# Kernel tuning notes

Hardware: AMD Instinct MI355X
Metric: run time of the kernel (lower is better)

## Reference

```python
import jax, jax.numpy as jnp
import numpy as np


def _conv(x, w, b=None, stride=1, pad=1, groups=1):
    y = jax.lax.conv_general_dilated(
        x, w, (stride, stride), [(pad, pad), (pad, pad)],
        dimension_numbers=('NCHW', 'OIHW', 'NCHW'), feature_group_count=groups)
    return y if b is None else y + b[None, :, None, None]


def _dwt(x):
    # Haar DWT as grouped stride-2 conv, filters pre-flipped as in the torch code
    ll = np.array([[0.5, 0.5], [0.5, 0.5]])
    lh = np.array([[-0.5, -0.5], [0.5, 0.5]])
    hl = np.array([[-0.5, 0.5], [-0.5, 0.5]])
    hh = np.array([[0.5, -0.5], [-0.5, 0.5]])
    filts = np.stack([f[None, ::-1, ::-1] for f in (ll, lh, hl, hh)], 0)  # [4,1,2,2]
    w = jnp.asarray(np.concatenate([filts] * 3, 0), x.dtype)  # [12,1,2,2], groups=3
    return _conv(x, w, None, stride=2, pad=0, groups=3)


def setup_inputs():
    key = jax.random.key(0)
    ks = iter(jax.random.split(key, 64))
    def w(*shape):
        return jax.random.normal(next(ks), shape, jnp.float32) * 0.05
    B, H, W = 4, 512, 512
    F = 32  # number_f
    d = {'x': jax.random.uniform(next(ks), (B, 3, H, W), jnp.float32)}
    d['enc1_w'] = w(F, 3, 3, 3); d['enc1_b'] = w(F)
    for i in range(2, 6):
        d['enc%d_w' % i] = w(F, F, 3, 3); d['enc%d_b' % i] = w(F)
    d['cdc_w'] = w(F, F, 3, 3)                      # central-difference conv, no bias
    d['ct_w'] = w(64, 9, 3, 3); d['ct_b'] = w(64)   # conv_theta on 9-ch high_freq
    d['t1_w'] = w(64, 64, 1, 1); d['t1_b'] = w(64)
    d['t2_w'] = w(64, 64, 1, 1); d['t2_b'] = w(64)
    d['t3_w'] = w(1, 64, 1, 1); d['t3_b'] = w(1)
    d['lf_w'] = w(64, 3, 3, 3); d['lf_b'] = w(64)   # low_freq conv on haar_A
    d['fc1_w'] = w(512, 64); d['fc1_b'] = w(512)
    d['fc2_w'] = w(512, 512); d['fc2_b'] = w(512)
    d['fc3_w'] = w(512, 512); d['fc3_b'] = w(512)
    d['g_w'] = w(F, 512); d['g_b'] = w(F)           # to_gamma_0
    d['be_w'] = w(F, 512); d['be_b'] = w(F)         # to_beta_0
    d['res_w'] = w(F, F, 3, 3); d['res_b'] = w(F)
    d['d1_w'] = w(F, F, 3, 3); d['d1_b'] = w(F)
    d['d2_w'] = w(1, F, 3, 3); d['d2_b'] = w(1)
    return d


def reference(x, enc1_w, enc1_b, enc2_w, enc2_b, enc3_w, enc3_b, enc4_w, enc4_b,
              enc5_w, enc5_b, cdc_w, ct_w, ct_b, t1_w, t1_b, t2_w, t2_b, t3_w, t3_b,
              lf_w, lf_b, fc1_w, fc1_b, fc2_w, fc2_b, fc3_w, fc3_b,
              g_w, g_b, be_w, be_b, res_w, res_b, d1_w, d1_b, d2_w, d2_b):
    relu = jax.nn.relu
    # encoder
    f = relu(_conv(x, enc1_w, enc1_b))
    f = relu(_conv(f, enc2_w, enc2_b))
    f = relu(_conv(f, enc3_w, enc3_b))
    f = relu(_conv(f, enc4_w, enc4_b))
    f_org4 = relu(_conv(f, enc5_w, enc5_b))  # [B,32,H,W]
    # Haar wavelet split: per input channel blocks of 4 = (A,H,V,D)
    dwt = _dwt(x)                             # [B,12,H/2,W/2]
    haar_A = dwt[:, 0::4]                     # c1,c5,c9
    high_freq = jnp.concatenate([dwt[:, 1::4], dwt[:, 2::4], dwt[:, 3::4]], 1)  # [B,9,...]
    # theta net (Conv2d_cd)
    a = relu(_conv(high_freq, ct_w, ct_b))
    a = a.mean((2, 3), keepdims=True)         # adaptive avg pool to 1x1
    a = relu(_conv(a, t1_w, t1_b, pad=0))
    a = relu(_conv(a, t2_w, t2_b, pad=0))
    theta = jax.nn.sigmoid(_conv(a, t3_w, t3_b, pad=0))   # [B,1,1,1]
    out_normal = _conv(f_org4, cdc_w, None)
    kdiff = cdc_w.sum((2, 3))[:, :, None, None]            # [32,32,1,1]
    out_diff = _conv(f_org4, kdiff, None, pad=0)
    f_deco = relu(out_normal - theta * out_diff)           # [B,32,H,W]
    # attention / FiLM branch
    am = relu(_conv(haar_A, lf_w, lf_b)).mean((2, 3))      # [B,64]
    am = relu(am @ fc1_w.T + fc1_b)
    am = relu(am @ fc2_w.T + fc2_b)
    am = jax.nn.sigmoid(am @ fc3_w.T + fc3_b)              # [B,512]
    gamma = jax.nn.sigmoid(am @ g_w.T + g_b)[:, :, None, None]  # [B,32,1,1]
    beta = jnp.tanh(am @ be_w.T + be_b)[:, :, None, None]
    f = f_deco + gamma * _conv(f_deco, res_w, res_b) + beta
    # decoder
    f = relu(_conv(f, d1_w, d1_b))
    out_map = jnp.tanh(_conv(f, d2_w, d2_b))               # [B,1,H,W]
    enhance_image = x + out_map * (x * x - x)
    return enhance_image, out_map
```

## Files before the change

### kernel.cpp

```cpp
#include <hip/hip_runtime.h>
#include <hip/hip_bf16.h>
#include <cmath>

#define TPB 256

typedef __attribute__((ext_vector_type(8))) short s16x8;
typedef __attribute__((ext_vector_type(4))) float f32x4;
typedef unsigned short ushortT;

constexpr long long PSTR = 8454272;
constexpr int HW = 512 * 512;

static __device__ __forceinline__ short f2bf(float f) {
    union { __hip_bfloat16 h; short s; } u;
    u.h = __float2bfloat16(f);
    return u.s;
}
static __device__ __forceinline__ float bf2f(unsigned short u) {
    union { unsigned int i; float f; } v;
    v.i = ((unsigned int)u) << 16;
    return v.f;
}
static __device__ __forceinline__ unsigned int pack2(float a, float b) {
    return (unsigned int)(unsigned short)f2bf(a) | ((unsigned int)(unsigned short)f2bf(b) << 16);
}

#define GLOAD_LDS16(gp, lp) \
    __builtin_amdgcn_global_load_lds((const __attribute__((address_space(1))) void*)(gp), \
                                     (__attribute__((address_space(3))) void*)(lp), 16, 0, 0)

static __device__ void pack_body(const float* w, const float* bias, const float* theta,
                                 short* dst, int CO, int CI_src, int ci_off, int cog, int l)
{
    const int l15 = l & 15, sl = l >> 4;
    for (int t = 0; t < 9; ++t) {
        for (int mt = 0; mt < 2; ++mt) {
            const int co = cog * 32 + 16 * mt + l15;
            s16x8 p;
            #pragma unroll
            for (int i = 0; i < 8; ++i) {
                const int pci = 8 * sl + i;
                float val = 0.f;
                if (co < CO && pci >= ci_off && pci < ci_off + CI_src) {
                    const int ci = pci - ci_off;
                    val = w[((size_t)co * CI_src + ci) * 9 + t];
                    if (theta && t == 4) {
                        float s = 0.f;
                        for (int tt = 0; tt < 9; ++tt) s += w[((size_t)co * CI_src + ci) * 9 + tt];
                        val -= theta[0] * s;
                    }
                }
                p[i] = f2bf(val);
            }
            *(s16x8*)(dst + ((size_t)(t * 2 + mt) * 64 + l) * 8) = p;
        }
    }
    if (l < 32) {
        const int co = cog * 32 + l;
        ((float*)(dst + 9216))[l] = (bias && co < CO) ? bias[co] : 0.f;
    }
}

__global__ __launch_bounds__(64) void packall_k(
    const float* e1w, const float* e1b, const float* e2w, const float* e2b,
    const float* e3w, const float* e3b, const float* e4w, const float* e4b,
    const float* e5w, const float* e5b, const float* resw, const float* resb,
    const float* d1w, const float* d1b, const float* d2w, const float* d2b,
    const float* ctw, const float* ctb, const float* lfw, const float* lfb,
    short* wpack)
{
    const int s = blockIdx.x;
    const float *w, *b;
    int CO = 32, CI = 32, coff = 0, cog = 0;
    switch (s) {
        case 0: w = e1w; b = e1b; CI = 3; break;
        case 1: w = e2w; b = e2b; break;
        case 2: w = e3w; b = e3b; break;
        case 3: w = e4w; b = e4b; break;
        case 4: w = e5w; b = e5b; break;
        case 5: w = resw; b = resb; break;
        case 6: w = d1w; b = d1b; break;
        case 7: w = d2w; b = d2b; CO = 1; break;
        case 8: case 9: w = ctw; b = ctb; CO = 64; CI = 9; cog = s - 8; break;
        default: w = lfw; b = lfb; CO = 64; CI = 3; coff = 9; cog = s - 10; break;
    }
    pack_body(w, b, nullptr, wpack + (size_t)s * 10240, CO, CI, coff, cog, threadIdx.x);
}

__global__ __launch_bounds__(64) void packcdc_k(
    const float* cdcw, const float* theta, short* wpack)
{
    const int b = blockIdx.x;
    pack_body(cdcw, nullptr, theta + b, wpack + (size_t)(12 + b) * 10240, 32, 32, 0, 0, threadIdx.x);
}

__global__ __launch_bounds__(TPB) void zero_k(unsigned int* A2u, unsigned int* B2u)
{
    const int idx = blockIdx.x * TPB + threadIdx.x;
    if (idx >= 8 * 32832) return;
    const int q = idx / 32832, r = idx % 32832;
    unsigned int* P = (q < 4 ? A2u : B2u) + (size_t)(q & 3) * 4227136;
    const int RSU = 514 * 16;
    int off;
    if (r < 8224)       off = r;
    else if (r < 16448) off = 513 * RSU + (r - 8224);
    else if (r < 24640) { int u = r - 16448; off = (1 + (u >> 4)) * RSU + (u & 15); }
    else                { int u = r - 24640; off = (1 + (u >> 4)) * RSU + 513 * 16 + (u & 15); }
    P[off] = 0u;
}

__global__ __launch_bounds__(TPB) void ctlf_k(
    const float* __restrict__ hf0, const float* __restrict__ haarA0,
    const short* __restrict__ wpack8, float* __restrict__ part)
{
    constexpr int RSX = 66;
    constexpr int ROWB = RSX * 64;
    __shared__ s16x8 lds_t[6 * RSX * 4];
    __shared__ float s_red[4][32];
    char* sb = (char*)lds_t;

    const int z = blockIdx.z, cog = blockIdx.y;
    const int bid = blockIdx.x;
    const int x0 = (bid & 3) * 64, y0 = (bid >> 2) * 4;
    const int tid = threadIdx.x, lane = tid & 63, wv = tid >> 6;
    const int l15 = lane & 15, slot = lane >> 4;

    const short* wslot = wpack8 + (size_t)cog * 10240;
    const float* hfz = hf0 + (size_t)z * 9 * 65536;
    const float* haz = haarA0 + (size_t)z * 3 * 65536;

    s16x8 wf[9][2];
    #pragma unroll
    for (int t = 0; t < 9; ++t)
        #pragma unroll
        for (int mt = 0; mt < 2; ++mt)
            wf[t][mt] = *(const s16x8*)(wslot + ((size_t)(t * 2 + mt) * 64 + lane) * 8);

    #pragma unroll
    for (int j = 0; j < 7; ++j) {
        const int p = j * 256 + tid;
        if (p < 1584) {
            const int row = p / 264;
            const int rem = p - row * 264;
            const int lx = rem >> 2, osl = rem & 3;
            const int o = osl ^ ((lx + (lx >> 2)) & 3);
            s16x8 pk;
            #pragma unroll
            for (int i = 0; i < 8; ++i) pk[i] = 0;
            const int sy = y0 + row - 1, sx = x0 + lx - 1;
            if (o < 2 && sy >= 0 && sy < 256 && sx >= 0 && sx < 256) {
                const size_t base = (size_t)sy * 256 + sx;
                if (o == 0) {
                    #pragma unroll
                    for (int i = 0; i < 8; ++i)
                        pk[i] = f2bf(hfz[(size_t)i * 65536 + base]);
                } else {
                    pk[0] = f2bf(hfz[(size_t)8 * 65536 + base]);
                    pk[1] = f2bf(haz[base]);
                    pk[2] = f2bf(haz[(size_t)65536 + base]);
                    pk[3] = f2bf(haz[(size_t)2 * 65536 + base]);
                }
            }
            *(s16x8*)(sb + p * 16) = pk;
        }
    }
    __syncthreads();

    const int xw = 16 * wv;
    int roff[3];
    #pragma unroll
    for (int dx = 0; dx < 3; ++dx) {
        const int lx = xw + dx + l15;
        const int vs = (lx + (lx >> 2)) & 3;
        roff[dx] = lx * 64 + ((slot ^ vs) << 4);
    }
    const float* bptr = (const float*)(wslot + 9216);

    float ps[2][4];
    #pragma unroll
    for (int mt = 0; mt < 2; ++mt)
        #pragma unroll
        for (int reg = 0; reg < 4; ++reg) ps[mt][reg] = 0.f;

    #pragma unroll
    for (int r2 = 0; r2 < 4; r2 += 2) {
        f32x4 acc[2][2];
        #pragma unroll
        for (int a = 0; a < 2; ++a)
            #pragma unroll
            for (int b = 0; b < 2; ++b)
                #pragma unroll
                for (int e = 0; e < 4; ++e) acc[a][b][e] = 0.f;

        #pragma unroll
        for (int dy = 0; dy < 3; ++dy) {
            const int rb0 = (r2 + dy) * ROWB;
            #pragma unroll
            for (int dx = 0; dx < 3; ++dx) {
                const int tap = dy * 3 + dx;
                const s16x8 b0 = *(const s16x8*)(sb + rb0 + roff[dx]);
                const s16x8 b1 = *(const s16x8*)(sb + rb0 + ROWB + roff[dx]);
                #pragma unroll
                for (int mt = 0; mt < 2; ++mt) {
                    acc[0][mt] = __builtin_amdgcn_mfma_f32_16x16x32_bf16(wf[tap][mt], b0, acc[0][mt], 0, 0, 0);
                    acc[1][mt] = __builtin_amdgcn_mfma_f32_16x16x32_bf16(wf[tap][mt], b1, acc[1][mt], 0, 0, 0);
                }
            }
        }

        #pragma unroll
        for (int rr = 0; rr < 2; ++rr)
            #pragma unroll
            for (int mt = 0; mt < 2; ++mt)
                #pragma unroll
                for (int reg = 0; reg < 4; ++reg)
                    ps[mt][reg] += fmaxf(acc[rr][mt][reg] + bptr[16 * mt + 4 * slot + reg], 0.f);
    }

    #pragma unroll
    for (int mt = 0; mt < 2; ++mt)
        #pragma unroll
        for (int reg = 0; reg < 4; ++reg) {
            #pragma unroll
            for (int o = 1; o < 16; o <<= 1)
                ps[mt][reg] += __shfl_xor(ps[mt][reg], o, 64);
        }
    #pragma unroll
    for (int mt = 0; mt < 2; ++mt)
        #pragma unroll
        for (int reg = 0; reg < 4; ++reg)
            if (l15 == mt * 4 + reg)
                s_red[wv][16 * mt + 4 * slot + reg] = ps[mt][reg];
    __syncthreads();
    if (tid < 32) {
        const float s = s_red[0][tid] + s_red[1][tid] + s_red[2][tid] + s_red[3][tid];
        part[(((size_t)z * 4 + cog) * 256 + bid) * 32 + tid] = s;
    }
}

__global__ __launch_bounds__(TPB) void enc1n_k(
    const float* __restrict__ x0p, const short* __restrict__ wslot,
    ushortT* __restrict__ outP0)
{
    constexpr int RSX = 66;
    constexpr int ROWB = RSX * 64;
    __shared__ s16x8 lds_t[6 * RSX * 4];
    char* sb = (char*)lds_t;

    const int z = blockIdx.z;
    const float* xin = x0p + (size_t)z * 3 * HW;

    const int tid = threadIdx.x, lane = tid & 63, wv = tid >> 6;
    const int bid = blockIdx.x;
    const int swz = (bid & 7) * 128 + (bid >> 3);
    const int x0 = (swz & 7) * 64, y0 = (swz >> 3) * 4;
    const int l15 = lane & 15, slot = lane >> 4;

    s16x8 wf[9][2];
    #pragma unroll
    for (int t = 0; t < 9; ++t)
        #pragma unroll
        for (int mt = 0; mt < 2; ++mt)
            wf[t][mt] = *(const s16x8*)(wslot + ((size_t)(t * 2 + mt) * 64 + lane) * 8);

    #pragma unroll
    for (int j = 0; j < 7; ++j) {
        const int p = j * 256 + tid;
        if (p < 1584) {
            const int row = p / 264;
            const int rem = p - row * 264;
            const int lx = rem >> 2, osl = rem & 3;
            const int o = osl ^ ((lx + (lx >> 2)) & 3);
            s16x8 pk;
            #pragma unroll
            for (int i = 0; i < 8; ++i) pk[i] = 0;
            if (o == 0) {
                const int gy = y0 + row - 1;
                const int gx = x0 + lx - 1;
                if (gy >= 0 && gy < 512 && gx >= 0 && gx < 512) {
                    #pragma unroll
                    for (int c = 0; c < 3; ++c)
                        pk[c] = f2bf(xin[((size_t)c * 512 + gy) * 512 + gx]);
                }
            }
            *(s16x8*)(sb + p * 16) = pk;
        }
    }
    __syncthreads();

    const int xw = 16 * wv;
    int roff[3];
    #pragma unroll
    for (int dx = 0; dx < 3; ++dx) {
        const int lx = xw + dx + l15;
        const int vs = (lx + (lx >> 2)) & 3;
        roff[dx] = lx * 64 + ((slot ^ vs) << 4);
    }
    const float* bptr = (const float*)(wslot + 9216);
    ushortT* outP = outP0 + (size_t)z * PSTR;

    #pragma unroll
    for (int r2 = 0; r2 < 4; r2 += 2) {
        f32x4 acc[2][2];
        #pragma unroll
        for (int a = 0; a < 2; ++a)
            #pragma unroll
            for (int b = 0; b < 2; ++b)
                #pragma unroll
                for (int e = 0; e < 4; ++e) acc[a][b][e] = 0.f;

        #pragma unroll
        for (int dy = 0; dy < 3; ++dy) {
            const int rb0 = (r2 + dy) * ROWB;
            #pragma unroll
            for (int dx = 0; dx < 3; ++dx) {
                const int tap = dy * 3 + dx;
                const s16x8 b0 = *(const s16x8*)(sb + rb0 + roff[dx]);
                const s16x8 b1 = *(const s16x8*)(sb + rb0 + ROWB + roff[dx]);
                #pragma unroll
                for (int mt = 0; mt < 2; ++mt) {
                    acc[0][mt] = __builtin_amdgcn_mfma_f32_16x16x32_bf16(wf[tap][mt], b0, acc[0][mt], 0, 0, 0);
                    acc[1][mt] = __builtin_amdgcn_mfma_f32_16x16x32_bf16(wf[tap][mt], b1, acc[1][mt], 0, 0, 0);
                }
            }
        }

        #pragma unroll
        for (int rr = 0; rr < 2; ++rr) {
            const int gy = y0 + r2 + rr;
            const int gx = x0 + xw + l15;
            #pragma unroll
            for (int mt = 0; mt < 2; ++mt) {
                const size_t off = ((size_t)(gy + 1) * 514 + gx + 1) * 32 + 16 * mt + 4 * slot;
                float v[4];
                #pragma unroll
                for (int reg = 0; reg < 4; ++reg)
                    v[reg] = fmaxf(acc[rr][mt][reg] + bptr[16 * mt + 4 * slot + reg], 0.f);
                *(uint2*)(outP + off) = make_uint2(pack2(v[0], v[1]), pack2(v[2], v[3]));
            }
        }
    }
}

template<int EPI>
__global__ __launch_bounds__(TPB) void dconv64p_k(
    const ushortT* __restrict__ inP0, const short* __restrict__ wbase, int wstr,
    ushortT* __restrict__ outP0,
    const float* __restrict__ gamma0, const float* __restrict__ beta0,
    const float* __restrict__ xorig0, float* __restrict__ outE0, float* __restrict__ outM0)
{
    constexpr int MT = (EPI == 3) ? 1 : 2;
    constexpr int RSX = 66;
    constexpr int ROWB = RSX * 64;
    constexpr int BUFB = 6 * RSX * 64;
    __shared__ s16x8 lds_t[2 * 6 * RSX * 4];
    char* sbase = (char*)lds_t;

    const int z = blockIdx.z;
    const ushortT* inP = inP0 + (size_t)z * PSTR;
    const short* wslot = wbase + (size_t)z * wstr;

    const int tid = threadIdx.x, lane = tid & 63, wv = tid >> 6;
    const int bid = blockIdx.x;
    const int xcd = bid & 7, idx = bid >> 3;
    const int x0 = (idx & 7) * 64;
    const int yband = xcd * 4 + (idx >> 3);
    const int l15 = lane & 15, slot = lane >> 4;

    s16x8 wf[9][MT];
    #pragma unroll
    for (int t = 0; t < 9; ++t)
        #pragma unroll
        for (int mt = 0; mt < MT; ++mt)
            wf[t][mt] = *(const s16x8*)(wslot + ((size_t)(t * 2 + mt) * 64 + lane) * 8);

    const int xw = 16 * wv;
    int roff[3];
    #pragma unroll
    for (int dx = 0; dx < 3; ++dx) {
        const int lx = xw + dx + l15;
        const int vs = (lx + (lx >> 2)) & 3;
        roff[dx] = lx * 64 + ((slot ^ vs) << 4);
    }
    const float* bptr = (const float*)(wslot + 9216);

    auto stage = [&](int t, int b) {
        const int y0 = yband * 16 + 4 * t;
        char* sb = sbase + b * BUFB;
        #pragma unroll
        for (int j = 0; j < 6; ++j) {
            const int p = j * 256 + tid;
            const int row = p / 264;
            const int rem = p - row * 264;
            const int lx = rem >> 2, osl = rem & 3;
            const int o = osl ^ ((lx + (lx >> 2)) & 3);
            const ushortT* gp = inP + ((size_t)(y0 + row) * 514 + x0 + lx) * 32 + o * 8;
            GLOAD_LDS16(gp, sb + (size_t)(j * 256 + wv * 64) * 16);
        }
        if (tid < 48) {
            const int p = 1536 + tid;
            const int row = p / 264;
            const int rem = p - row * 264;
            const int lx = rem >> 2, osl = rem & 3;
            const int o = osl ^ ((lx + (lx >> 2)) & 3);
            const ushortT* gp = inP + ((size_t)(y0 + row) * 514 + x0 + lx) * 32 + o * 8;
            GLOAD_LDS16(gp, sb + (size_t)1536 * 16);
        }
    };

    stage(0, 0);

    #pragma unroll 1
    for (int t = 0; t < 4; ++t) {
        __syncthreads();
        if (t < 3) stage(t + 1, (t + 1) & 1);
        char* sb = sbase + (t & 1) * BUFB;
        const int y0t = yband * 16 + 4 * t;

        #pragma unroll
        for (int r2 = 0; r2 < 4; r2 += 2) {
            f32x4 acc[2][MT];
            #pragma unroll
            for (int a = 0; a < 2; ++a)
                #pragma unroll
                for (int b = 0; b < MT; ++b)
                    #pragma unroll
                    for (int e = 0; e < 4; ++e) acc[a][b][e] = 0.f;

            #pragma unroll
            for (int dy = 0; dy < 3; ++dy) {
                const int rb0 = (r2 + dy) * ROWB;
                #pragma unroll
                for (int dx = 0; dx < 3; ++dx) {
                    const int tap = dy * 3 + dx;
                    const s16x8 b0 = *(const s16x8*)(sb + rb0 + roff[dx]);
                    const s16x8 b1 = *(const s16x8*)(sb + rb0 + ROWB + roff[dx]);
                    #pragma unroll
                    for (int mt = 0; mt < MT; ++mt) {
                        acc[0][mt] = __builtin_amdgcn_mfma_f32_16x16x32_bf16(wf[tap][mt], b0, acc[0][mt], 0, 0, 0);
                        acc[1][mt] = __builtin_amdgcn_mfma_f32_16x16x32_bf16(wf[tap][mt], b1, acc[1][mt], 0, 0, 0);
                    }
                }
            }

            #pragma unroll
            for (int rr = 0; rr < 2; ++rr) {
                const int gy = y0t + r2 + rr;
                const int gx = x0 + xw + l15;
                if constexpr (EPI == 3) {
                    if (slot == 0) {
                        const float* xorig = xorig0 + (size_t)z * 3 * HW;
                        float* outE = outE0 + (size_t)z * 3 * HW;
                        float* outM = outM0 + (size_t)z * HW;
                        const float om = tanhf(acc[rr][0][0] + bptr[0]);
                        outM[(size_t)gy * 512 + gx] = om;
                        #pragma unroll
                        for (int c = 0; c < 3; ++c) {
                            const size_t xi = ((size_t)c * 512 + gy) * 512 + gx;
                            const float xv = xorig[xi];
                            outE[xi] = xv + om * (xv * xv - xv);
                        }
                    }
                } else {
                    ushortT* outP = outP0 + (size_t)z * PSTR;
                    #pragma unroll
                    for (int mt = 0; mt < MT; ++mt) {
                        const size_t off = ((size_t)(gy + 1) * 514 + gx + 1) * 32 + 16 * mt + 4 * slot;
                        float v[4];
                        #pragma unroll
                        for (int reg = 0; reg < 4; ++reg)
                            v[reg] = acc[rr][mt][reg] + bptr[16 * mt + 4 * slot + reg];
                        if constexpr (EPI == 0) {
                            #pragma unroll
                            for (int reg = 0; reg < 4; ++reg) v[reg] = fmaxf(v[reg], 0.f);
                        } else if constexpr (EPI == 2) {
                            const int prow = r2 + rr + 1;
                            const int lxr = xw + l15 + 1;
                            const int vsr = (lxr + (lxr >> 2)) & 3;
                            const int oo = (2 * mt + (slot >> 1)) ^ vsr;
                            const uint2 din = *(const uint2*)(sb + (prow * RSX + lxr) * 64 + (oo << 4) + ((slot & 1) << 3));
                            const float* gamma = gamma0 + 32 * z;
                            const float* beta  = beta0 + 32 * z;
                            const int cb = 16 * mt + 4 * slot;
                            v[0] = bf2f((unsigned short)(din.x & 0xffff)) + gamma[cb + 0] * v[0] + beta[cb + 0];
                            v[1] = bf2f((unsigned short)(din.x >> 16))    + gamma[cb + 1] * v[1] + beta[cb + 1];
                            v[2] = bf2f((unsigned short)(din.y & 0xffff)) + gamma[cb + 2] * v[2] + beta[cb + 2];
                            v[3] = bf2f((unsigned short)(din.y >> 16))    + gamma[cb + 3] * v[3] + beta[cb + 3];
                        }
                        *(uint2*)(outP + off) = make_uint2(pack2(v[0], v[1]), pack2(v[2], v[3]));
                    }
                }
            }
        }
    }
}

__global__ __launch_bounds__(TPB) void dwt_k(
    const float* __restrict__ x, float* __restrict__ haarA, float* __restrict__ hf)
{
    const int idx = blockIdx.x * TPB + threadIdx.x;
    if (idx >= 4 * 256 * 256) return;
    const int xo = idx & 255;
    const int yo = (idx >> 8) & 255;
    const int b  = idx >> 16;
    #pragma unroll
    for (int c = 0; c < 3; ++c) {
        const float* p = x + (((size_t)b * 3 + c) * 512 + 2 * yo) * 512 + 2 * xo;
        const float a = p[0], bb = p[1], cc = p[512], d = p[513];
        haarA[(((size_t)b * 3 + c) * 256 + yo) * 256 + xo] = 0.5f * (a + bb + cc + d);
        hf[(((size_t)b * 9 + 0 + c) * 256 + yo) * 256 + xo] = 0.5f * (a + bb - cc - d);
        hf[(((size_t)b * 9 + 3 + c) * 256 + yo) * 256 + xo] = 0.5f * (a - bb + cc - d);
        hf[(((size_t)b * 9 + 6 + c) * 256 + yo) * 256 + xo] = 0.5f * (a - bb - cc + d);
    }
}

__global__ __launch_bounds__(TPB) void meanfin_k(
    const float* __restrict__ part, float* __restrict__ amean, float* __restrict__ am0)
{
    const int br = blockIdx.x;
    const int o = threadIdx.x;
    const int z = o >> 6, co = o & 63;
    const int cog = (br ? 2 : 0) + (co >> 5), c = co & 31;
    const float* p = part + (((size_t)z * 4 + cog) * 256) * 32 + c;
    float s = 0.f;
    for (int j = 0; j < 256; ++j) s += p[j * 32];
    (br ? am0 : amean)[z * 64 + co] = s * (1.f / 65536.f);
}

__global__ __launch_bounds__(64) void tchain_k(
    const float* __restrict__ amean,
    const float* __restrict__ t1w, const float* __restrict__ t1b,
    const float* __restrict__ t2w, const float* __restrict__ t2b,
    const float* __restrict__ t3w, const float* __restrict__ t3b,
    float* __restrict__ theta)
{
    const int b = blockIdx.x;
    const float* am = amean + b * 64;
    __shared__ float a0[64], a1[64], a2[64];
    const int co = threadIdx.x;
    a0[co] = am[co];
    __syncthreads();
    float s = t1b[co];
    #pragma unroll 8
    for (int ci = 0; ci < 64; ++ci) s = fmaf(t1w[co * 64 + ci], a0[ci], s);
    a1[co] = fmaxf(s, 0.f);
    __syncthreads();
    s = t2b[co];
    #pragma unroll 8
    for (int ci = 0; ci < 64; ++ci) s = fmaf(t2w[co * 64 + ci], a1[ci], s);
    a2[co] = fmaxf(s, 0.f);
    __syncthreads();
    if (co == 0) {
        float v = t3b[0];
        for (int ci = 0; ci < 64; ++ci) v = fmaf(t3w[ci], a2[ci], v);
        theta[b] = 1.f / (1.f + expf(-v));
    }
}

template<int ACT>
__global__ __launch_bounds__(TPB) void fcw_k(
    const float* __restrict__ in, const float* __restrict__ w,
    const float* __restrict__ bias, float* __restrict__ out, int K, int N)
{
    const int lane = threadIdx.x & 63, wv = threadIdx.x >> 6;
    const int idx = blockIdx.x * 4 + wv;
    if (idx >= 4 * N) return;
    const int b = idx / N, co = idx % N;
    float s = 0.f;
    for (int k = lane * 4; k < K; k += 256) {
        const float4 wv4 = *(const float4*)(w + (size_t)co * K + k);
        const float4 iv  = *(const float4*)(in + (size_t)b * K + k);
        s += wv4.x * iv.x + wv4.y * iv.y + wv4.z * iv.z + wv4.w * iv.w;
    }
    #pragma unroll
    for (int o = 32; o > 0; o >>= 1) s += __shfl_xor(s, o, 64);
    if (lane == 0) {
        s += bias[co];
        if (ACT == 0) s = fmaxf(s, 0.f);
        else if (ACT == 1) s = 1.f / (1.f + expf(-s));
        else s = tanhf(s);
        out[(size_t)b * N + co] = s;
    }
}

extern "C" void kernel_launch(void* const* d_in, const int* in_sizes, int n_in,
                              void* d_out, int out_size, void* d_ws, size_t ws_size,
                              hipStream_t stream)
{
    const float* x      = (const float*)d_in[0];
    const float* cdc_w  = (const float*)d_in[11];
    const float* t1_w   = (const float*)d_in[14];
    const float* t1_b   = (const float*)d_in[15];
    const float* t2_w   = (const float*)d_in[16];
    const float* t2_b   = (const float*)d_in[17];
    const float* t3_w   = (const float*)d_in[18];
    const float* t3_b   = (const float*)d_in[19];
    const float* fc1_w  = (const float*)d_in[22];
    const float* fc1_b  = (const float*)d_in[23];
    const float* fc2_w  = (const float*)d_in[24];
    const float* fc2_b  = (const float*)d_in[25];
    const float* fc3_w  = (const float*)d_in[26];
    const float* fc3_b  = (const float*)d_in[27];
    const float* g_w    = (const float*)d_in[28];
    const float* g_b    = (const float*)d_in[29];
    const float* be_w   = (const float*)d_in[30];
    const float* be_b   = (const float*)d_in[31];

    float* out = (float*)d_out;

    ushortT* A2 = (ushortT*)d_ws;
    ushortT* B2 = A2 + 4 * PSTR;
    float* haarA = (float*)B2;
    float* hf    = haarA + 786432;
    float* part  = (float*)(B2 + 4 * PSTR);
    float* amean = part + 131072;
    float* am0   = amean + 256;
    float* am1   = am0 + 256;
    float* am2   = am1 + 2048;
    float* am3   = am2 + 2048;
    float* theta = am3 + 2048;
    float* gamma = theta + 4;
    float* beta  = gamma + 128;
    short* wpack = (short*)(beta + 128);
    const size_t need_bytes = (size_t)((char*)(wpack + 16 * 10240) - (char*)d_ws);
    if (ws_size < need_bytes) return;

    const dim3 blk(TPB);

    dwt_k<<<dim3((4 * 256 * 256 + TPB - 1) / TPB), blk, 0, stream>>>(x, haarA, hf);
    packall_k<<<dim3(12), dim3(64), 0, stream>>>(
        (const float*)d_in[1], (const float*)d_in[2], (const float*)d_in[3], (const float*)d_in[4],
        (const float*)d_in[5], (const float*)d_in[6], (const float*)d_in[7], (const float*)d_in[8],
        (const float*)d_in[9], (const float*)d_in[10], (const float*)d_in[32], (const float*)d_in[33],
        (const float*)d_in[34], (const float*)d_in[35], (const float*)d_in[36], (const float*)d_in[37],
        (const float*)d_in[12], (const float*)d_in[13], (const float*)d_in[20], (const float*)d_in[21],
        wpack);

    ctlf_k<<<dim3(256, 4, 4), blk, 0, stream>>>(hf, haarA, wpack + 8 * 10240, part);

    zero_k<<<dim3((8 * 32832 + TPB - 1) / TPB), blk, 0, stream>>>((unsigned int*)A2, (unsigned int*)B2);

    meanfin_k<<<dim3(2), blk, 0, stream>>>(part, amean, am0);
    tchain_k<<<dim3(4), dim3(64), 0, stream>>>(amean, t1_w, t1_b, t2_w, t2_b, t3_w, t3_b, theta);
    fcw_k<0><<<dim3(512), blk, 0, stream>>>(am0, fc1_w, fc1_b, am1, 64, 512);
    fcw_k<0><<<dim3(512), blk, 0, stream>>>(am1, fc2_w, fc2_b, am2, 512, 512);
    fcw_k<1><<<dim3(512), blk, 0, stream>>>(am2, fc3_w, fc3_b, am3, 512, 512);
    fcw_k<1><<<dim3(32), blk, 0, stream>>>(am3, g_w, g_b, gamma, 512, 32);
    fcw_k<2><<<dim3(32), blk, 0, stream>>>(am3, be_w, be_b, beta, 512, 32);
    packcdc_k<<<dim3(4), dim3(64), 0, stream>>>(cdc_w, theta, wpack);

    const dim3 gE(1024, 1, 4);
    const dim3 gP(256, 1, 4);
    float* outM = out + (size_t)4 * 3 * HW;

    enc1n_k<<<gE, blk, 0, stream>>>(x, wpack, A2);
    dconv64p_k<0><<<gP, blk, 0, stream>>>(A2, wpack + 1 * 10240, 0, B2, nullptr, nullptr, nullptr, nullptr, nullptr);
    dconv64p_k<0><<<gP, blk, 0, stream>>>(B2, wpack + 2 * 10240, 0, A2, nullptr, nullptr, nullptr, nullptr, nullptr);
    dconv64p_k<0><<<gP, blk, 0, stream>>>(A2, wpack + 3 * 10240, 0, B2, nullptr, nullptr, nullptr, nullptr, nullptr);
    dconv64p_k<0><<<gP, blk, 0, stream>>>(B2, wpack + 4 * 10240, 0, A2, nullptr, nullptr, nullptr, nullptr, nullptr);
    dconv64p_k<0><<<gP, blk, 0, stream>>>(A2, wpack + 12 * 10240, 10240, B2, nullptr, nullptr, nullptr, nullptr, nullptr);
    dconv64p_k<2><<<gP, blk, 0, stream>>>(B2, wpack + 5 * 10240, 0, A2, gamma, beta, nullptr, nullptr, nullptr);
    dconv64p_k<0><<<gP, blk, 0, stream>>>(A2, wpack + 6 * 10240, 0, B2, nullptr, nullptr, nullptr, nullptr, nullptr);
    dconv64p_k<3><<<gP, blk, 0, stream>>>(B2, wpack + 7 * 10240, 0, nullptr, nullptr, nullptr, x, out, outM);
}
```

Measured before the change: 364.7 us.

## Fuse Haar DWT into ctlf conv staging and simplify LDS tile loads

```diff
diff --git a/kernel.cpp b/kernel.cpp
--- a/kernel.cpp
+++ b/kernel.cpp
@@ -110,8 +110,8 @@
 }
 
 __global__ __launch_bounds__(TPB) void ctlf_k(
-    const float* __restrict__ hf0, const float* __restrict__ haarA0,
-    const short* __restrict__ wpack8, float* __restrict__ part)
+    const float* __restrict__ x0p, const short* __restrict__ wpack8,
+    float* __restrict__ part)
 {
     constexpr int RSX = 66;
     constexpr int ROWB = RSX * 64;
@@ -126,8 +126,7 @@
     const int l15 = lane & 15, slot = lane >> 4;
 
     const short* wslot = wpack8 + (size_t)cog * 10240;
-    const float* hfz = hf0 + (size_t)z * 9 * 65536;
-    const float* haz = haarA0 + (size_t)z * 3 * 65536;
+    const float* xz = x0p + (size_t)z * 3 * HW;
 
     s16x8 wf[9][2];
     #pragma unroll
@@ -137,31 +136,36 @@
             wf[t][mt] = *(const s16x8*)(wslot + ((size_t)(t * 2 + mt) * 64 + lane) * 8);
 
     #pragma unroll
-    for (int j = 0; j < 7; ++j) {
+    for (int j = 0; j < 2; ++j) {
         const int p = j * 256 + tid;
-        if (p < 1584) {
-            const int row = p / 264;
-            const int rem = p - row * 264;
-            const int lx = rem >> 2, osl = rem & 3;
-            const int o = osl ^ ((lx + (lx >> 2)) & 3);
-            s16x8 pk;
-            #pragma unroll
-            for (int i = 0; i < 8; ++i) pk[i] = 0;
+        if (p < 396) {
+            const int row = p / 66, lx = p - row * 66;
+            const int vs = (lx + (lx >> 2)) & 3;
+            char* base = sb + (row * RSX + lx) * 64;
             const int sy = y0 + row - 1, sx = x0 + lx - 1;
-            if (o < 2 && sy >= 0 && sy < 256 && sx >= 0 && sx < 256) {
-                const size_t base = (size_t)sy * 256 + sx;
-                if (o == 0) {
-                    #pragma unroll
-                    for (int i = 0; i < 8; ++i)
-                        pk[i] = f2bf(hfz[(size_t)i * 65536 + base]);
-                } else {
-                    pk[0] = f2bf(hfz[(size_t)8 * 65536 + base]);
-                    pk[1] = f2bf(haz[base]);
-                    pk[2] = f2bf(haz[(size_t)65536 + base]);
-                    pk[3] = f2bf(haz[(size_t)2 * 65536 + base]);
+            s16x8 pk0, pk1, zz;
+            #pragma unroll
+            for (int i = 0; i < 8; ++i) { pk0[i] = 0; pk1[i] = 0; zz[i] = 0; }
+            if (sy >= 0 && sy < 256 && sx >= 0 && sx < 256) {
+                #pragma unroll
+                for (int c = 0; c < 3; ++c) {
+                    const float* xp = xz + ((size_t)c * 512 + 2 * sy) * 512 + 2 * sx;
+                    const float2 tp = *(const float2*)xp;
+                    const float2 bt = *(const float2*)(xp + 512);
+                    const float a = tp.x, b = tp.y, cc = bt.x, d = bt.y;
+                    pk0[c]     = f2bf(0.5f * (a + b - cc - d));
+                    pk0[3 + c] = f2bf(0.5f * (a - b + cc - d));
+                    const float hh = 0.5f * (a - b - cc + d);
+                    const float ll = 0.5f * (a + b + cc + d);
+                    if (c < 2) pk0[6 + c] = f2bf(hh);
+                    else       pk1[0]     = f2bf(hh);
+                    pk1[1 + c] = f2bf(ll);
                 }
             }
-            *(s16x8*)(sb + p * 16) = pk;
+            *(s16x8*)(base + ((0 ^ vs) << 4)) = pk0;
+            *(s16x8*)(base + ((1 ^ vs) << 4)) = pk1;
+            *(s16x8*)(base + ((2 ^ vs) << 4)) = zz;
+            *(s16x8*)(base + ((3 ^ vs) << 4)) = zz;
         }
     }
     __syncthreads();
@@ -264,26 +268,25 @@
             wf[t][mt] = *(const s16x8*)(wslot + ((size_t)(t * 2 + mt) * 64 + lane) * 8);
 
     #pragma unroll
-    for (int j = 0; j < 7; ++j) {
+    for (int j = 0; j < 2; ++j) {
         const int p = j * 256 + tid;
-        if (p < 1584) {
-            const int row = p / 264;
-            const int rem = p - row * 264;
-            const int lx = rem >> 2, osl = rem & 3;
-            const int o = osl ^ ((lx + (lx >> 2)) & 3);
-            s16x8 pk;
-            #pragma unroll
-            for (int i = 0; i < 8; ++i) pk[i] = 0;
-            if (o == 0) {
-                const int gy = y0 + row - 1;
-                const int gx = x0 + lx - 1;
-                if (gy >= 0 && gy < 512 && gx >= 0 && gx < 512) {
-                    #pragma unroll
-                    for (int c = 0; c < 3; ++c)
-                        pk[c] = f2bf(xin[((size_t)c * 512 + gy) * 512 + gx]);
-                }
-            }
-            *(s16x8*)(sb + p * 16) = pk;
+        if (p < 396) {
+            const int row = p / 66, lx = p - row * 66;
+            const int vs = (lx + (lx >> 2)) & 3;
+            char* base = sb + (row * RSX + lx) * 64;
+            const int gy = y0 + row - 1, gx = x0 + lx - 1;
+            s16x8 pk, zz;
+            #pragma unroll
+            for (int i = 0; i < 8; ++i) { pk[i] = 0; zz[i] = 0; }
+            if (gy >= 0 && gy < 512 && gx >= 0 && gx < 512) {
+                #pragma unroll
+                for (int c = 0; c < 3; ++c)
+                    pk[c] = f2bf(xin[((size_t)c * 512 + gy) * 512 + gx]);
+            }
+            *(s16x8*)(base + ((0 ^ vs) << 4)) = pk;
+            *(s16x8*)(base + ((1 ^ vs) << 4)) = zz;
+            *(s16x8*)(base + ((2 ^ vs) << 4)) = zz;
+            *(s16x8*)(base + ((3 ^ vs) << 4)) = zz;
         }
     }
     __syncthreads();
@@ -495,25 +498,6 @@
     }
 }
 
-__global__ __launch_bounds__(TPB) void dwt_k(
-    const float* __restrict__ x, float* __restrict__ haarA, float* __restrict__ hf)
-{
-    const int idx = blockIdx.x * TPB + threadIdx.x;
-    if (idx >= 4 * 256 * 256) return;
-    const int xo = idx & 255;
-    const int yo = (idx >> 8) & 255;
-    const int b  = idx >> 16;
-    #pragma unroll
-    for (int c = 0; c < 3; ++c) {
-        const float* p = x + (((size_t)b * 3 + c) * 512 + 2 * yo) * 512 + 2 * xo;
-        const float a = p[0], bb = p[1], cc = p[512], d = p[513];
-        haarA[(((size_t)b * 3 + c) * 256 + yo) * 256 + xo] = 0.5f * (a + bb + cc + d);
-        hf[(((size_t)b * 9 + 0 + c) * 256 + yo) * 256 + xo] = 0.5f * (a + bb - cc - d);
-        hf[(((size_t)b * 9 + 3 + c) * 256 + yo) * 256 + xo] = 0.5f * (a - bb + cc - d);
-        hf[(((size_t)b * 9 + 6 + c) * 256 + yo) * 256 + xo] = 0.5f * (a - bb - cc + d);
-    }
-}
-
 __global__ __launch_bounds__(TPB) void meanfin_k(
     const float* __restrict__ part, float* __restrict__ amean, float* __restrict__ am0)
 {
@@ -610,8 +594,6 @@
 
     ushortT* A2 = (ushortT*)d_ws;
     ushortT* B2 = A2 + 4 * PSTR;
-    float* haarA = (float*)B2;
-    float* hf    = haarA + 786432;
     float* part  = (float*)(B2 + 4 * PSTR);
     float* amean = part + 131072;
     float* am0   = amean + 256;
@@ -627,7 +609,6 @@
 
     const dim3 blk(TPB);
 
-    dwt_k<<<dim3((4 * 256 * 256 + TPB - 1) / TPB), blk, 0, stream>>>(x, haarA, hf);
     packall_k<<<dim3(12), dim3(64), 0, stream>>>(
         (const float*)d_in[1], (const float*)d_in[2], (const float*)d_in[3], (const float*)d_in[4],
         (const float*)d_in[5], (const float*)d_in[6], (const float*)d_in[7], (const float*)d_in[8],
@@ -636,9 +617,9 @@
         (const float*)d_in[12], (const float*)d_in[13], (const float*)d_in[20], (const float*)d_in[21],
         wpack);
 
-    ctlf_k<<<dim3(256, 4, 4), blk, 0, stream>>>(hf, haarA, wpack + 8 * 10240, part);
-
     zero_k<<<dim3((8 * 32832 + TPB - 1) / TPB), blk, 0, stream>>>((unsigned int*)A2, (unsigned int*)B2);
+
+    ctlf_k<<<dim3(256, 4, 4), blk, 0, stream>>>(x, wpack + 8 * 10240, part);
 
     meanfin_k<<<dim3(2), blk, 0, stream>>>(part, amean, am0);
     tchain_k<<<dim3(4), dim3(64), 0, stream>>>(amean, t1_w, t1_b, t2_w, t2_b, t3_w, t3_b, theta);
```

Result: faster. 332.5 us (-8.8%).
